# Optimization experiments

Hardware: AMD Instinct MI355X
Metric: run time of the kernel (lower is better)

## Reference

```python
import jax, jax.numpy as jnp
import numpy as np


def _quantize_activation(x):
    """Vectorized equivalent of improved_quantize_activation.

    Original per-element loop: scale by dynamic percentile-based scale, floor,
    clamp to int8 range, take two's-complement 8-bit string, replace the low
    4 bits with '1000', then MSR-4 'compensation' sets the last bit to '1'
    (unconditionally in both branches) -> low nibble becomes 0b1001 = 9.
    Equivalent bit ops: u = (q mod 256) & 0xF0 | 0x09, re-sign, dequantize.
    The torch code detaches (numpy round-trip), so gradients are cut; we
    mirror that with stop_gradient.
    """
    flat = x.reshape(-1)
    abs_max = jnp.maximum(jnp.abs(jnp.percentile(flat, 2.5)),
                          jnp.abs(jnp.percentile(flat, 97.5)))
    scale = jnp.where(abs_max > 0, 127.0 / abs_max, 128.0)
    q = jnp.clip(jnp.floor(x * scale), -128.0, 127.0).astype(jnp.int32)
    u = jnp.mod(q, 256)                      # two's complement byte
    u2 = jnp.bitwise_or(jnp.bitwise_and(u, 0xF0), 9)  # low nibble -> 1001
    s = jnp.where(u2 >= 128, u2 - 256, u2)   # back to signed int8 value
    return jax.lax.stop_gradient(s.astype(x.dtype) / scale)


def _conv2d(x, w, b, pad):
    y = jax.lax.conv_general_dilated(
        x, w, window_strides=(1, 1), padding=[(pad, pad), (pad, pad)],
        dimension_numbers=('NCHW', 'OIHW', 'NCHW'))
    return y + b[None, :, None, None]


def _maxpool2(x):
    return jax.lax.reduce_window(x, -jnp.inf, jax.lax.max,
                                 (1, 1, 2, 2), (1, 1, 2, 2), 'VALID')


def setup_inputs() -> dict:
    key = jax.random.key(0)
    ks = jax.random.split(key, 11)
    B = 16384
    x = jax.random.normal(ks[0], (B, 1, 28, 28), dtype=jnp.float32)
    def u(k, shape, fan_in):
        bound = 1.0 / np.sqrt(fan_in)
        return jax.random.uniform(k, shape, jnp.float32, -bound, bound)
    return {
        'x': x,
        'conv1_w': u(ks[1], (6, 1, 5, 5), 1 * 25),
        'conv1_b': u(ks[2], (6,), 1 * 25),
        'conv2_w': u(ks[3], (16, 6, 5, 5), 6 * 25),
        'conv2_b': u(ks[4], (16,), 6 * 25),
        'fc1_w': u(ks[5], (120, 400), 400),
        'fc1_b': u(ks[6], (120,), 400),
        'fc2_w': u(ks[7], (84, 120), 120),
        'fc2_b': u(ks[8], (84,), 120),
        'fc3_w': u(ks[9], (10, 84), 84),
        'fc3_b': u(ks[10], (10,), 84),
    }


def reference(x, conv1_w, conv1_b, conv2_w, conv2_b,
              fc1_w, fc1_b, fc2_w, fc2_b, fc3_w, fc3_b):
    h = jax.nn.relu(_conv2d(x, conv1_w, conv1_b, pad=2))   # [B,6,28,28]
    h = _maxpool2(h)                                       # [B,6,14,14]
    h = _quantize_activation(h)
    h = jax.nn.relu(_conv2d(h, conv2_w, conv2_b, pad=0))   # [B,16,10,10]
    h = _maxpool2(h)                                       # [B,16,5,5]
    h = _quantize_activation(h)
    h = h.reshape(h.shape[0], -1)                          # [B,400]
    h = jax.nn.relu(h @ fc1_w.T + fc1_b)
    h = _quantize_activation(h)
    # dropout is identity in eval mode
    h = jax.nn.relu(h @ fc2_w.T + fc2_b)
    h = _quantize_activation(h)
    return h @ fc3_w.T + fc3_b                             # [B,10]
```

## Files before the change

### kernel.cpp

```cpp
#include <hip/hip_runtime.h>
#include <stdint.h>
#include <math.h>

#define NB 16384

struct Ctrl {
  unsigned rank[4];
  unsigned key[4];
  float scale;
  unsigned pad[7];
};
static_assert(sizeof(Ctrl) == 64, "ctrl size");

__device__ __forceinline__ unsigned keyOf(float x) {
  unsigned u = __float_as_uint(x);
  return (u & 0x80000000u) ? ~u : (u | 0x80000000u);
}
__device__ __forceinline__ float keyToFloat(unsigned k) {
  unsigned u = (k & 0x80000000u) ? (k ^ 0x80000000u) : ~k;
  return __uint_as_float(u);
}

__global__ __launch_bounds__(256) void conv1_pool(
    const float* __restrict__ x, const float* __restrict__ w,
    const float* __restrict__ bias, float* __restrict__ out) {
  __shared__ float img[784];
  __shared__ float wl[150];
  __shared__ float bl[6];
  int t = threadIdx.x;
  int b = blockIdx.x;
  const float* xb = x + (size_t)b * 784;
  for (int i = t; i < 784; i += 256) img[i] = xb[i];
  if (t < 150) wl[t] = w[t];
  if (t < 6) bl[t] = bias[t];
  __syncthreads();
  for (int o = t; o < 1176; o += 256) {
    int c = o / 196;
    int rem = o % 196;
    int r = rem / 14, col = rem % 14;
    float win[6][6];
    int r0 = 2 * r - 2, c0 = 2 * col - 2;
#pragma unroll
    for (int i = 0; i < 6; i++) {
      int rr = r0 + i;
#pragma unroll
      for (int j = 0; j < 6; j++) {
        int cc = c0 + j;
        win[i][j] = (rr >= 0 && rr < 28 && cc >= 0 && cc < 28) ? img[rr * 28 + cc] : 0.0f;
      }
    }
    float s00 = 0.f, s01 = 0.f, s10 = 0.f, s11 = 0.f;
    const float* wc = &wl[c * 25];
#pragma unroll
    for (int i = 0; i < 5; i++) {
#pragma unroll
      for (int j = 0; j < 5; j++) {
        float wv = wc[i * 5 + j];
        s00 = fmaf(win[i][j], wv, s00);
        s01 = fmaf(win[i][j + 1], wv, s01);
        s10 = fmaf(win[i + 1][j], wv, s10);
        s11 = fmaf(win[i + 1][j + 1], wv, s11);
      }
    }
    float m = fmaxf(fmaxf(s00, s01), fmaxf(s10, s11));
    out[(size_t)b * 1176 + o] = fmaxf(m + bl[c], 0.0f);
  }
}

__global__ __launch_bounds__(256) void conv2_pool(
    const float* __restrict__ a, const float* __restrict__ w,
    const float* __restrict__ bias, float* __restrict__ out) {
  __shared__ float img[1176];
  __shared__ float wl[2400];
  __shared__ float bl[16];
  int t = threadIdx.x;
  int b = blockIdx.x;
  const float* ab = a + (size_t)b * 1176;
  for (int i = t; i < 1176; i += 256) img[i] = ab[i];
  for (int i = t; i < 2400; i += 256) wl[i] = w[i];
  if (t < 16) bl[t] = bias[t];
  __syncthreads();
  for (int o = t; o < 400; o += 256) {
    int c = o / 25;
    int rem = o % 25;
    int r = rem / 5, col = rem % 5;
    float s00 = 0.f, s01 = 0.f, s10 = 0.f, s11 = 0.f;
    for (int ci = 0; ci < 6; ci++) {
      float win[6][6];
      const float* ic = &img[ci * 196 + (2 * r) * 14 + 2 * col];
#pragma unroll
      for (int i = 0; i < 6; i++)
#pragma unroll
        for (int j = 0; j < 6; j++) win[i][j] = ic[i * 14 + j];
      const float* wc = &wl[(c * 6 + ci) * 25];
#pragma unroll
      for (int i = 0; i < 5; i++) {
#pragma unroll
        for (int j = 0; j < 5; j++) {
          float wv = wc[i * 5 + j];
          s00 = fmaf(win[i][j], wv, s00);
          s01 = fmaf(win[i][j + 1], wv, s01);
          s10 = fmaf(win[i + 1][j], wv, s10);
          s11 = fmaf(win[i + 1][j + 1], wv, s11);
        }
      }
    }
    float m = fmaxf(fmaxf(s00, s01), fmaxf(s10, s11));
    out[(size_t)b * 400 + o] = fmaxf(m + bl[c], 0.0f);
  }
}

__global__ __launch_bounds__(256) void hist_top(
    const float4* __restrict__ a, long long n4, unsigned* __restrict__ hist) {
  __shared__ unsigned h[4096];
  int t = threadIdx.x;
  for (int i = t; i < 4096; i += 256) h[i] = 0;
  __syncthreads();
  long long stride = (long long)gridDim.x * 256;
  for (long long i = (long long)blockIdx.x * 256 + t; i < n4; i += stride) {
    float4 v = a[i];
    atomicAdd(&h[keyOf(v.x) >> 20], 1u);
    atomicAdd(&h[keyOf(v.y) >> 20], 1u);
    atomicAdd(&h[keyOf(v.z) >> 20], 1u);
    atomicAdd(&h[keyOf(v.w) >> 20], 1u);
  }
  __syncthreads();
  for (int i = t; i < 4096; i += 256) {
    unsigned v = h[i];
    if (v) atomicAdd(&hist[i], v);
  }
}

__global__ __launch_bounds__(256) void hist_sub(
    const float4* __restrict__ a, long long n4, const Ctrl* __restrict__ c,
    unsigned* __restrict__ hist, int level) {
  __shared__ unsigned h[4096];
  int t = threadIdx.x;
  for (int i = t; i < 4096; i += 256) h[i] = 0;
  __syncthreads();
  unsigned p0 = c->key[0], p1 = c->key[1], p2 = c->key[2], p3 = c->key[3];
  unsigned mask = (level == 2) ? 0xFFF00000u : 0xFFFFFC00u;
  int sh = (level == 2) ? 10 : 0;
  long long stride = (long long)gridDim.x * 256;
  for (long long i = (long long)blockIdx.x * 256 + t; i < n4; i += stride) {
    float4 v = a[i];
    float vals[4] = {v.x, v.y, v.z, v.w};
#pragma unroll
    for (int q = 0; q < 4; q++) {
      unsigned k = keyOf(vals[q]);
      unsigned pf = k & mask;
      unsigned bin = (k >> sh) & 1023u;
      if (pf == p0) atomicAdd(&h[bin], 1u);
      if (pf == p1) atomicAdd(&h[1024 + bin], 1u);
      if (pf == p2) atomicAdd(&h[2048 + bin], 1u);
      if (pf == p3) atomicAdd(&h[3072 + bin], 1u);
    }
  }
  __syncthreads();
  for (int i = t; i < 4096; i += 256) {
    unsigned v = h[i];
    if (v) atomicAdd(&hist[i], v);
  }
}

__global__ __launch_bounds__(256) void scan_step(
    const unsigned* __restrict__ hist, int nbins, int sharedHist, int shift,
    Ctrl* __restrict__ c, int first, unsigned r0, unsigned r1, unsigned r2,
    unsigned r3, int finalize, float lwlo, float hwlo, float lwhi, float hwhi) {
  __shared__ unsigned base[256];
  int t = threadIdx.x;
  unsigned rinit[4] = {r0, r1, r2, r3};
  int per = nbins / 256;
  for (int j = 0; j < 4; j++) {
    const unsigned* h = hist + (sharedHist ? 0 : j * nbins);
    unsigned s = 0;
    for (int i = 0; i < per; i++) s += h[t * per + i];
    base[t] = s;
    __syncthreads();
    if (t == 0) {
      unsigned acc = 0;
      for (int i = 0; i < 256; i++) {
        unsigned v = base[i];
        base[i] = acc;
        acc += v;
      }
    }
    __syncthreads();
    unsigned rank = first ? rinit[j] : c->rank[j];
    unsigned bexc = base[t];
    if (rank >= bexc && rank < bexc + s) {
      unsigned cum = bexc;
      for (int i = 0; i < per; i++) {
        unsigned cnt = h[t * per + i];
        if (rank < cum + cnt) {
          c->rank[j] = rank - cum;
          c->key[j] |= ((unsigned)(t * per + i)) << shift;
          break;
        }
        cum += cnt;
      }
    }
    __syncthreads();
  }
  if (finalize && t == 0) {
    float v0 = keyToFloat(c->key[0]), v1 = keyToFloat(c->key[1]);
    float v2 = keyToFloat(c->key[2]), v3 = keyToFloat(c->key[3]);
    float plo = __fadd_rn(__fmul_rn(v0, lwlo), __fmul_rn(v1, hwlo));
    float phi = __fadd_rn(__fmul_rn(v2, lwhi), __fmul_rn(v3, hwhi));
    float am = fmaxf(fabsf(plo), fabsf(phi));
    c->scale = (am > 0.0f) ? __fdiv_rn(127.0f, am) : 128.0f;
  }
}

__device__ __forceinline__ float qmap1(float x, float scale) {
  float t = __fmul_rn(x, scale);
  t = floorf(t);
  t = fminf(fmaxf(t, -128.0f), 127.0f);
  int qi = (int)t;
  int u2 = (qi & 0xF0) | 9;
  int s = (u2 >= 128) ? (u2 - 256) : u2;
  return __fdiv_rn((float)s, scale);
}

__global__ __launch_bounds__(256) void quant_map(
    float4* __restrict__ a, long long n4, const Ctrl* __restrict__ c) {
  float scale = c->scale;
  long long stride = (long long)gridDim.x * 256;
  for (long long i = (long long)blockIdx.x * 256 + threadIdx.x; i < n4; i += stride) {
    float4 v = a[i];
    v.x = qmap1(v.x, scale);
    v.y = qmap1(v.y, scale);
    v.z = qmap1(v.z, scale);
    v.w = qmap1(v.w, scale);
    a[i] = v;
  }
}

__global__ __launch_bounds__(256) void fc1_kernel(
    const float* __restrict__ A, const float* __restrict__ W,
    const float* __restrict__ bias, float* __restrict__ out) {
  __shared__ float As[32][100];
  __shared__ float Ws[120][100];
  int t = threadIdx.x;
  size_t b0 = (size_t)blockIdx.x * 32;
  int ng = t & 7, bs = t >> 3;
  float acc[15];
#pragma unroll
  for (int i = 0; i < 15; i++) acc[i] = 0.f;
  for (int kc = 0; kc < 4; kc++) {
    for (int idx = t; idx < 3200; idx += 256) {
      int row = idx / 100, k = idx % 100;
      As[row][k] = A[(b0 + row) * 400 + kc * 100 + k];
    }
    for (int idx = t; idx < 12000; idx += 256) {
      int n = idx / 100, k = idx % 100;
      Ws[n][k] = W[n * 400 + kc * 100 + k];
    }
    __syncthreads();
    for (int k = 0; k < 100; k++) {
      float av = As[bs][k];
#pragma unroll
      for (int i = 0; i < 15; i++) acc[i] = fmaf(av, Ws[ng + 8 * i][k], acc[i]);
    }
    __syncthreads();
  }
#pragma unroll
  for (int i = 0; i < 15; i++) {
    int n = ng + 8 * i;
    out[(b0 + bs) * 120 + n] = fmaxf(acc[i] + bias[n], 0.0f);
  }
}

__global__ __launch_bounds__(256) void fc2_kernel(
    const float* __restrict__ A, const float* __restrict__ W,
    const float* __restrict__ bias, float* __restrict__ out) {
  __shared__ float As[64][121];
  __shared__ float Ws[84][120];
  int t = threadIdx.x;
  size_t b0 = (size_t)blockIdx.x * 64;
  int ng = t & 3, bs = t >> 2;
  float acc[21];
#pragma unroll
  for (int i = 0; i < 21; i++) acc[i] = 0.f;
  for (int idx = t; idx < 7680; idx += 256) {
    int row = idx / 120, k = idx % 120;
    As[row][k] = A[(b0 + row) * 120 + k];
  }
  for (int idx = t; idx < 10080; idx += 256) {
    int n = idx / 120, k = idx % 120;
    Ws[n][k] = W[n * 120 + k];
  }
  __syncthreads();
  for (int k = 0; k < 120; k++) {
    float av = As[bs][k];
#pragma unroll
    for (int i = 0; i < 21; i++) acc[i] = fmaf(av, Ws[ng + 4 * i][k], acc[i]);
  }
#pragma unroll
  for (int i = 0; i < 21; i++) {
    int n = ng + 4 * i;
    out[(b0 + bs) * 84 + n] = fmaxf(acc[i] + bias[n], 0.0f);
  }
}

__global__ __launch_bounds__(256) void fc3_kernel(
    const float* __restrict__ A, const float* __restrict__ W,
    const float* __restrict__ bias, float* __restrict__ out) {
  __shared__ float As[64][84];
  __shared__ float Ws[10][84];
  __shared__ float bl[10];
  int t = threadIdx.x;
  size_t b0 = (size_t)blockIdx.x * 64;
  int ng = t & 3, bs = t >> 2;
  for (int idx = t; idx < 5376; idx += 256) {
    int row = idx / 84, k = idx % 84;
    As[row][k] = A[(b0 + row) * 84 + k];
  }
  for (int idx = t; idx < 840; idx += 256) Ws[idx / 84][idx % 84] = W[idx];
  if (t < 10) bl[t] = bias[t];
  __syncthreads();
  float acc[3] = {0.f, 0.f, 0.f};
  for (int k = 0; k < 84; k++) {
    float av = As[bs][k];
#pragma unroll
    for (int i = 0; i < 3; i++) {
      int n = ng + 4 * i;
      if (n < 10) acc[i] = fmaf(av, Ws[n][k], acc[i]);
    }
  }
#pragma unroll
  for (int i = 0; i < 3; i++) {
    int n = ng + 4 * i;
    if (n < 10) out[(b0 + bs) * 10 + n] = acc[i] + bl[n];
  }
}

static void qparams(long long n, unsigned r[4], float w[4]) {
  float nf = (float)n;
  float nm1 = nf - 1.0f;
  float qlo = 2.5f / 100.0f, qhi = 97.5f / 100.0f;
  float ilo = qlo * nm1;
  float flo = floorf(ilo), clo = ceilf(ilo);
  float hwlo = ilo - flo, lwlo = 1.0f - hwlo;
  float ihi = qhi * nm1;
  float fhi = floorf(ihi), chi = ceilf(ihi);
  float hwhi = ihi - fhi, lwhi = 1.0f - hwhi;
  if (flo < 0) flo = 0;
  if (clo < 0) clo = 0;
  if (fhi < 0) fhi = 0;
  if (chi < 0) chi = 0;
  unsigned nmax = (unsigned)(n - 1);
  r[0] = (unsigned)flo; if (r[0] > nmax) r[0] = nmax;
  r[1] = (unsigned)clo; if (r[1] > nmax) r[1] = nmax;
  r[2] = (unsigned)fhi; if (r[2] > nmax) r[2] = nmax;
  r[3] = (unsigned)chi; if (r[3] > nmax) r[3] = nmax;
  w[0] = lwlo; w[1] = hwlo; w[2] = lwhi; w[3] = hwhi;
}

extern "C" void kernel_launch(void* const* d_in, const int* in_sizes, int n_in,
                              void* d_out, int out_size, void* d_ws, size_t ws_size,
                              hipStream_t stream) {
  const float* x   = (const float*)d_in[0];
  const float* c1w = (const float*)d_in[1];
  const float* c1b = (const float*)d_in[2];
  const float* c2w = (const float*)d_in[3];
  const float* c2b = (const float*)d_in[4];
  const float* f1w = (const float*)d_in[5];
  const float* f1b = (const float*)d_in[6];
  const float* f2w = (const float*)d_in[7];
  const float* f2b = (const float*)d_in[8];
  const float* f3w = (const float*)d_in[9];
  const float* f3b = (const float*)d_in[10];
  float* outp = (float*)d_out;

  char* ws = (char*)d_ws;
  size_t off = 0;
  auto alloc = [&](size_t bytes) {
    void* p = ws + off;
    off += (bytes + 255) & ~(size_t)255;
    return p;
  };
  float* act1 = (float*)alloc((size_t)NB * 1176 * 4);
  float* act2 = (float*)alloc((size_t)NB * 400 * 4);
  unsigned* hist1 = (unsigned*)alloc(4096 * 4);
  unsigned* hist2 = (unsigned*)alloc(4096 * 4);
  unsigned* hist3 = (unsigned*)alloc(4096 * 4);
  Ctrl* ctrl = (Ctrl*)alloc(sizeof(Ctrl));
  float* fc1o = act1;
  float* fc2o = act1 + (size_t)NB * 120;

  const int HB = 2048;

  auto runQuant = [&](float* act, long long n) {
    unsigned r[4];
    float w[4];
    qparams(n, r, w);
    hipMemsetAsync(hist1, 0, 3 * 4096 * 4 + sizeof(Ctrl), stream);
    long long n4 = n / 4;
    hist_top<<<HB, 256, 0, stream>>>((const float4*)act, n4, hist1);
    scan_step<<<1, 256, 0, stream>>>(hist1, 4096, 1, 20, ctrl, 1,
                                     r[0], r[1], r[2], r[3], 0, 0.f, 0.f, 0.f, 0.f);
    hist_sub<<<HB, 256, 0, stream>>>((const float4*)act, n4, ctrl, hist2, 2);
    scan_step<<<1, 256, 0, stream>>>(hist2, 1024, 0, 10, ctrl, 0,
                                     0u, 0u, 0u, 0u, 0, 0.f, 0.f, 0.f, 0.f);
    hist_sub<<<HB, 256, 0, stream>>>((const float4*)act, n4, ctrl, hist3, 3);
    scan_step<<<1, 256, 0, stream>>>(hist3, 1024, 0, 0, ctrl, 0,
                                     0u, 0u, 0u, 0u, 1, w[0], w[1], w[2], w[3]);
    quant_map<<<HB, 256, 0, stream>>>((float4*)act, n4, ctrl);
  };

  conv1_pool<<<NB, 256, 0, stream>>>(x, c1w, c1b, act1);
  runQuant(act1, (long long)NB * 1176);
  conv2_pool<<<NB, 256, 0, stream>>>(act1, c2w, c2b, act2);
  runQuant(act2, (long long)NB * 400);
  fc1_kernel<<<NB / 32, 256, 0, stream>>>(act2, f1w, f1b, fc1o);
  runQuant(fc1o, (long long)NB * 120);
  fc2_kernel<<<NB / 64, 256, 0, stream>>>(fc1o, f2w, f2b, fc2o);
  runQuant(fc2o, (long long)NB * 84);
  fc3_kernel<<<NB / 64, 256, 0, stream>>>(fc2o, f3w, f3b, outp);
}
```

Baseline: 1.082 ms.

## Fuse quantile histograms, scans and quant-map into conv/fc kernels with last-block scans

The top-level histogram is now built inside the producing conv/fc kernels, and each scan runs in the last block to finish, found through an atomic counter. This removes separate histogram and scan launches. The quantize-map pass is folded into the consumer kernel's input load, so there is no extra read/write pass over each activation. The conv kernels are also restructured: several images per block, padded shared tiles, two channels per thread in conv1, and register-blocked rows with transposed weights in conv2. Zero values are counted separately to avoid atomic contention on the many ReLU zeros. The cost is heavier kernels with more shared memory and last-block serialization of the scans.

```diff
diff --git a/kernel.cpp b/kernel.cpp
--- a/kernel.cpp
+++ b/kernel.cpp
@@ -20,198 +20,6 @@
   unsigned u = (k & 0x80000000u) ? (k ^ 0x80000000u) : ~k;
   return __uint_as_float(u);
 }
-
-__global__ __launch_bounds__(256) void conv1_pool(
-    const float* __restrict__ x, const float* __restrict__ w,
-    const float* __restrict__ bias, float* __restrict__ out) {
-  __shared__ float img[784];
-  __shared__ float wl[150];
-  __shared__ float bl[6];
-  int t = threadIdx.x;
-  int b = blockIdx.x;
-  const float* xb = x + (size_t)b * 784;
-  for (int i = t; i < 784; i += 256) img[i] = xb[i];
-  if (t < 150) wl[t] = w[t];
-  if (t < 6) bl[t] = bias[t];
-  __syncthreads();
-  for (int o = t; o < 1176; o += 256) {
-    int c = o / 196;
-    int rem = o % 196;
-    int r = rem / 14, col = rem % 14;
-    float win[6][6];
-    int r0 = 2 * r - 2, c0 = 2 * col - 2;
-#pragma unroll
-    for (int i = 0; i < 6; i++) {
-      int rr = r0 + i;
-#pragma unroll
-      for (int j = 0; j < 6; j++) {
-        int cc = c0 + j;
-        win[i][j] = (rr >= 0 && rr < 28 && cc >= 0 && cc < 28) ? img[rr * 28 + cc] : 0.0f;
-      }
-    }
-    float s00 = 0.f, s01 = 0.f, s10 = 0.f, s11 = 0.f;
-    const float* wc = &wl[c * 25];
-#pragma unroll
-    for (int i = 0; i < 5; i++) {
-#pragma unroll
-      for (int j = 0; j < 5; j++) {
-        float wv = wc[i * 5 + j];
-        s00 = fmaf(win[i][j], wv, s00);
-        s01 = fmaf(win[i][j + 1], wv, s01);
-        s10 = fmaf(win[i + 1][j], wv, s10);
-        s11 = fmaf(win[i + 1][j + 1], wv, s11);
-      }
-    }
-    float m = fmaxf(fmaxf(s00, s01), fmaxf(s10, s11));
-    out[(size_t)b * 1176 + o] = fmaxf(m + bl[c], 0.0f);
-  }
-}
-
-__global__ __launch_bounds__(256) void conv2_pool(
-    const float* __restrict__ a, const float* __restrict__ w,
-    const float* __restrict__ bias, float* __restrict__ out) {
-  __shared__ float img[1176];
-  __shared__ float wl[2400];
-  __shared__ float bl[16];
-  int t = threadIdx.x;
-  int b = blockIdx.x;
-  const float* ab = a + (size_t)b * 1176;
-  for (int i = t; i < 1176; i += 256) img[i] = ab[i];
-  for (int i = t; i < 2400; i += 256) wl[i] = w[i];
-  if (t < 16) bl[t] = bias[t];
-  __syncthreads();
-  for (int o = t; o < 400; o += 256) {
-    int c = o / 25;
-    int rem = o % 25;
-    int r = rem / 5, col = rem % 5;
-    float s00 = 0.f, s01 = 0.f, s10 = 0.f, s11 = 0.f;
-    for (int ci = 0; ci < 6; ci++) {
-      float win[6][6];
-      const float* ic = &img[ci * 196 + (2 * r) * 14 + 2 * col];
-#pragma unroll
-      for (int i = 0; i < 6; i++)
-#pragma unroll
-        for (int j = 0; j < 6; j++) win[i][j] = ic[i * 14 + j];
-      const float* wc = &wl[(c * 6 + ci) * 25];
-#pragma unroll
-      for (int i = 0; i < 5; i++) {
-#pragma unroll
-        for (int j = 0; j < 5; j++) {
-          float wv = wc[i * 5 + j];
-          s00 = fmaf(win[i][j], wv, s00);
-          s01 = fmaf(win[i][j + 1], wv, s01);
-          s10 = fmaf(win[i + 1][j], wv, s10);
-          s11 = fmaf(win[i + 1][j + 1], wv, s11);
-        }
-      }
-    }
-    float m = fmaxf(fmaxf(s00, s01), fmaxf(s10, s11));
-    out[(size_t)b * 400 + o] = fmaxf(m + bl[c], 0.0f);
-  }
-}
-
-__global__ __launch_bounds__(256) void hist_top(
-    const float4* __restrict__ a, long long n4, unsigned* __restrict__ hist) {
-  __shared__ unsigned h[4096];
-  int t = threadIdx.x;
-  for (int i = t; i < 4096; i += 256) h[i] = 0;
-  __syncthreads();
-  long long stride = (long long)gridDim.x * 256;
-  for (long long i = (long long)blockIdx.x * 256 + t; i < n4; i += stride) {
-    float4 v = a[i];
-    atomicAdd(&h[keyOf(v.x) >> 20], 1u);
-    atomicAdd(&h[keyOf(v.y) >> 20], 1u);
-    atomicAdd(&h[keyOf(v.z) >> 20], 1u);
-    atomicAdd(&h[keyOf(v.w) >> 20], 1u);
-  }
-  __syncthreads();
-  for (int i = t; i < 4096; i += 256) {
-    unsigned v = h[i];
-    if (v) atomicAdd(&hist[i], v);
-  }
-}
-
-__global__ __launch_bounds__(256) void hist_sub(
-    const float4* __restrict__ a, long long n4, const Ctrl* __restrict__ c,
-    unsigned* __restrict__ hist, int level) {
-  __shared__ unsigned h[4096];
-  int t = threadIdx.x;
-  for (int i = t; i < 4096; i += 256) h[i] = 0;
-  __syncthreads();
-  unsigned p0 = c->key[0], p1 = c->key[1], p2 = c->key[2], p3 = c->key[3];
-  unsigned mask = (level == 2) ? 0xFFF00000u : 0xFFFFFC00u;
-  int sh = (level == 2) ? 10 : 0;
-  long long stride = (long long)gridDim.x * 256;
-  for (long long i = (long long)blockIdx.x * 256 + t; i < n4; i += stride) {
-    float4 v = a[i];
-    float vals[4] = {v.x, v.y, v.z, v.w};
-#pragma unroll
-    for (int q = 0; q < 4; q++) {
-      unsigned k = keyOf(vals[q]);
-      unsigned pf = k & mask;
-      unsigned bin = (k >> sh) & 1023u;
-      if (pf == p0) atomicAdd(&h[bin], 1u);
-      if (pf == p1) atomicAdd(&h[1024 + bin], 1u);
-      if (pf == p2) atomicAdd(&h[2048 + bin], 1u);
-      if (pf == p3) atomicAdd(&h[3072 + bin], 1u);
-    }
-  }
-  __syncthreads();
-  for (int i = t; i < 4096; i += 256) {
-    unsigned v = h[i];
-    if (v) atomicAdd(&hist[i], v);
-  }
-}
-
-__global__ __launch_bounds__(256) void scan_step(
-    const unsigned* __restrict__ hist, int nbins, int sharedHist, int shift,
-    Ctrl* __restrict__ c, int first, unsigned r0, unsigned r1, unsigned r2,
-    unsigned r3, int finalize, float lwlo, float hwlo, float lwhi, float hwhi) {
-  __shared__ unsigned base[256];
-  int t = threadIdx.x;
-  unsigned rinit[4] = {r0, r1, r2, r3};
-  int per = nbins / 256;
-  for (int j = 0; j < 4; j++) {
-    const unsigned* h = hist + (sharedHist ? 0 : j * nbins);
-    unsigned s = 0;
-    for (int i = 0; i < per; i++) s += h[t * per + i];
-    base[t] = s;
-    __syncthreads();
-    if (t == 0) {
-      unsigned acc = 0;
-      for (int i = 0; i < 256; i++) {
-        unsigned v = base[i];
-        base[i] = acc;
-        acc += v;
-      }
-    }
-    __syncthreads();
-    unsigned rank = first ? rinit[j] : c->rank[j];
-    unsigned bexc = base[t];
-    if (rank >= bexc && rank < bexc + s) {
-      unsigned cum = bexc;
-      for (int i = 0; i < per; i++) {
-        unsigned cnt = h[t * per + i];
-        if (rank < cum + cnt) {
-          c->rank[j] = rank - cum;
-          c->key[j] |= ((unsigned)(t * per + i)) << shift;
-          break;
-        }
-        cum += cnt;
-      }
-    }
-    __syncthreads();
-  }
-  if (finalize && t == 0) {
-    float v0 = keyToFloat(c->key[0]), v1 = keyToFloat(c->key[1]);
-    float v2 = keyToFloat(c->key[2]), v3 = keyToFloat(c->key[3]);
-    float plo = __fadd_rn(__fmul_rn(v0, lwlo), __fmul_rn(v1, hwlo));
-    float phi = __fadd_rn(__fmul_rn(v2, lwhi), __fmul_rn(v3, hwhi));
-    float am = fmaxf(fabsf(plo), fabsf(phi));
-    c->scale = (am > 0.0f) ? __fdiv_rn(127.0f, am) : 128.0f;
-  }
-}
-
 __device__ __forceinline__ float qmap1(float x, float scale) {
   float t = __fmul_rn(x, scale);
   t = floorf(t);
@@ -221,36 +29,328 @@
   int s = (u2 >= 128) ? (u2 - 256) : u2;
   return __fdiv_rn((float)s, scale);
 }
-
-__global__ __launch_bounds__(256) void quant_map(
-    float4* __restrict__ a, long long n4, const Ctrl* __restrict__ c) {
-  float scale = c->scale;
+__device__ __forceinline__ unsigned loadAgent(const unsigned* p) {
+  return __hip_atomic_load(p, __ATOMIC_RELAXED, __HIP_MEMORY_SCOPE_AGENT);
+}
+__device__ __forceinline__ void load16(float* r, const float* p) {
+#pragma unroll
+  for (int s = 0; s < 4; s++) {
+    float4 f = *(const float4*)&p[4 * s];
+    r[4 * s] = f.x; r[4 * s + 1] = f.y; r[4 * s + 2] = f.z; r[4 * s + 3] = f.w;
+  }
+}
+
+__device__ void scan_device(const unsigned* hist, int nbins, int sharedHist, int shift,
+                            Ctrl* c, int first, unsigned r0, unsigned r1, unsigned r2,
+                            unsigned r3, int finalize, float lwlo, float hwlo,
+                            float lwhi, float hwhi, unsigned* base) {
+  int t = threadIdx.x;
+  unsigned rinit[4] = {r0, r1, r2, r3};
+  int per = nbins / 256;
+  for (int j = 0; j < 4; j++) {
+    const unsigned* h = hist + (sharedHist ? 0 : j * nbins);
+    unsigned s = 0;
+    for (int i = 0; i < per; i++) s += loadAgent(&h[t * per + i]);
+    base[t] = s;
+    __syncthreads();
+    if (t == 0) {
+      unsigned acc = 0;
+      for (int i = 0; i < 256; i++) { unsigned v = base[i]; base[i] = acc; acc += v; }
+    }
+    __syncthreads();
+    unsigned rank = first ? rinit[j] : c->rank[j];
+    unsigned bexc = base[t];
+    if (rank >= bexc && rank < bexc + s) {
+      unsigned cum = bexc;
+      for (int i = 0; i < per; i++) {
+        unsigned cnt = loadAgent(&h[t * per + i]);
+        if (rank < cum + cnt) {
+          c->rank[j] = rank - cum;
+          c->key[j] |= ((unsigned)(t * per + i)) << shift;
+          break;
+        }
+        cum += cnt;
+      }
+    }
+    __syncthreads();
+  }
+  if (finalize && t == 0) {
+    float v0 = keyToFloat(c->key[0]), v1 = keyToFloat(c->key[1]);
+    float v2 = keyToFloat(c->key[2]), v3 = keyToFloat(c->key[3]);
+    float plo = __fadd_rn(__fmul_rn(v0, lwlo), __fmul_rn(v1, hwlo));
+    float phi = __fadd_rn(__fmul_rn(v2, lwhi), __fmul_rn(v3, hwhi));
+    float am = fmaxf(fabsf(plo), fabsf(phi));
+    c->scale = (am > 0.0f) ? __fdiv_rn(127.0f, am) : 128.0f;
+  }
+}
+
+#define C1_IMGS 6
+__global__ __launch_bounds__(256) void conv1_fused(
+    const float* __restrict__ x, const float* __restrict__ w,
+    const float* __restrict__ bias, float* __restrict__ act1,
+    unsigned* __restrict__ hist, unsigned* __restrict__ counter, Ctrl* ctrl,
+    unsigned r0, unsigned r1, unsigned r2, unsigned r3) {
+  __shared__ __align__(16) float img[C1_IMGS * 1032];
+  __shared__ float wl[150];
+  __shared__ float bl[6];
+  __shared__ unsigned h[4096];
+  __shared__ unsigned sbase[256];
+  __shared__ unsigned lastFlag;
+  int t = threadIdx.x;
+  long long b0 = (long long)blockIdx.x * C1_IMGS;
+  for (int i = t; i < 4096; i += 256) h[i] = 0;
+  if (t < 150) wl[t] = w[t];
+  if (t < 6) bl[t] = bias[t];
+  for (int i = t; i < C1_IMGS * 1032; i += 256) img[i] = 0.0f;
+  __syncthreads();
+  for (int idx = t; idx < C1_IMGS * 784; idx += 256) {
+    int im = idx / 784, rem = idx % 784;
+    int r = rem / 28, cc = rem % 28;
+    long long bb = b0 + im;
+    if (bb < NB) img[im * 1032 + (r + 2) * 32 + (cc + 2)] = x[bb * 784 + rem];
+  }
+  __syncthreads();
+  unsigned zc = 0;
+  int im = t / 42, rem2 = t % 42, cg = rem2 / 14, pc = rem2 % 14;
+  if (im < C1_IMGS) {
+    long long bb = b0 + im;
+    if (bb < NB) {
+      const float* ib = &img[im * 1032];
+      float wa[25], wb[25];
+#pragma unroll
+      for (int k = 0; k < 25; k++) {
+        wa[k] = wl[(2 * cg) * 25 + k];
+        wb[k] = wl[(2 * cg + 1) * 25 + k];
+      }
+      float biasA = bl[2 * cg], biasB = bl[2 * cg + 1];
+      float* oA = act1 + bb * 1176 + (2 * cg) * 196 + pc;
+      float* oB = oA + 196;
+      for (int pr = 0; pr < 14; pr++) {
+        float rw[6][6];
+        const float* rp = ib + (2 * pr) * 32 + 2 * pc;
+#pragma unroll
+        for (int rr = 0; rr < 6; rr++) {
+#pragma unroll
+          for (int k2 = 0; k2 < 3; k2++) {
+            float2 f = *(const float2*)&rp[rr * 32 + 2 * k2];
+            rw[rr][2 * k2] = f.x;
+            rw[rr][2 * k2 + 1] = f.y;
+          }
+        }
+        float a00 = 0.f, a01 = 0.f, a10 = 0.f, a11 = 0.f;
+        float c00 = 0.f, c01 = 0.f, c10 = 0.f, c11 = 0.f;
+#pragma unroll
+        for (int i = 0; i < 5; i++) {
+#pragma unroll
+          for (int j = 0; j < 5; j++) {
+            float wva = wa[i * 5 + j], wvb = wb[i * 5 + j];
+            a00 = fmaf(rw[i][j], wva, a00);
+            a01 = fmaf(rw[i][j + 1], wva, a01);
+            a10 = fmaf(rw[i + 1][j], wva, a10);
+            a11 = fmaf(rw[i + 1][j + 1], wva, a11);
+            c00 = fmaf(rw[i][j], wvb, c00);
+            c01 = fmaf(rw[i][j + 1], wvb, c01);
+            c10 = fmaf(rw[i + 1][j], wvb, c10);
+            c11 = fmaf(rw[i + 1][j + 1], wvb, c11);
+          }
+        }
+        float ma = fmaxf(fmaxf(a00, a01), fmaxf(a10, a11));
+        float mb = fmaxf(fmaxf(c00, c01), fmaxf(c10, c11));
+        float va = fmaxf(ma + biasA, 0.0f);
+        float vb = fmaxf(mb + biasB, 0.0f);
+        oA[pr * 14] = va;
+        oB[pr * 14] = vb;
+        unsigned ba = __float_as_uint(va), bbit = __float_as_uint(vb);
+        if (ba == 0u) zc++; else atomicAdd(&h[keyOf(va) >> 20], 1u);
+        if (bbit == 0u) zc++; else atomicAdd(&h[keyOf(vb) >> 20], 1u);
+      }
+    }
+  }
+  if (zc) atomicAdd(&h[2048], zc);
+  __syncthreads();
+  for (int i = t; i < 4096; i += 256) {
+    unsigned v = h[i];
+    if (v) atomicAdd(&hist[i], v);
+  }
+  __threadfence();
+  if (t == 0) lastFlag = (atomicAdd(counter, 1u) == gridDim.x - 1);
+  __syncthreads();
+  if (lastFlag)
+    scan_device(hist, 4096, 1, 20, ctrl, 1, r0, r1, r2, r3, 0, 0.f, 0.f, 0.f, 0.f, sbase);
+}
+
+#define C2_IMGS 3
+__global__ __launch_bounds__(256) void conv2_fused(
+    const float* __restrict__ act1, const float* __restrict__ w,
+    const float* __restrict__ bias, const Ctrl* __restrict__ cin,
+    float* __restrict__ act2, unsigned* __restrict__ hist,
+    unsigned* __restrict__ counter, Ctrl* ctrl,
+    unsigned r0, unsigned r1, unsigned r2, unsigned r3) {
+  __shared__ __align__(16) float img[C2_IMGS * 1680];
+  __shared__ float wl[2400];
+  __shared__ float bl[16];
+  __shared__ unsigned h[4096];
+  __shared__ unsigned sbase[256];
+  __shared__ unsigned lastFlag;
+  int t = threadIdx.x;
+  long long b0 = (long long)blockIdx.x * C2_IMGS;
+  float scale = cin->scale;
+  for (int i = t; i < 4096; i += 256) h[i] = 0;
+  for (int idx = t; idx < 2400; idx += 256) {
+    int c = idx / 150, rem = idx % 150;
+    int ci = rem / 25, ki = (rem % 25) / 5, kj = rem % 5;
+    wl[((ci * 5 + ki) * 5 + kj) * 16 + c] = w[idx];
+  }
+  if (t < 16) bl[t] = bias[t];
+  for (int idx = t; idx < C2_IMGS * 1176; idx += 256) {
+    int im = idx / 1176, rem = idx % 1176;
+    int ci = rem / 196, rr = (rem % 196) / 14, cc = rem % 14;
+    long long bb = b0 + im;
+    float v = 0.0f;
+    if (bb < NB) v = qmap1(act1[bb * 1176 + rem], scale);
+    img[im * 1680 + ci * 280 + rr * 20 + cc] = v;
+  }
+  __syncthreads();
+  unsigned zc = 0;
+  int g = t >> 4;
+  int c = t & 15;
+  if (g < 15) {
+    int im = g / 5, pr = g % 5;
+    long long bb = b0 + im;
+    if (bb < NB) {
+      const float* ib = &img[im * 1680];
+      float acc0[10], acc1[10];
+#pragma unroll
+      for (int i = 0; i < 10; i++) { acc0[i] = 0.f; acc1[i] = 0.f; }
+      for (int ci = 0; ci < 6; ci++) {
+        const float* rbase = ib + ci * 280 + (2 * pr) * 20;
+        float ra[16], rb[16];
+        load16(ra, rbase);
+        load16(rb, rbase + 20);
+#pragma unroll
+        for (int ki = 0; ki < 5; ki++) {
+          float wv[5];
+#pragma unroll
+          for (int kj = 0; kj < 5; kj++) wv[kj] = wl[((ci * 5 + ki) * 5 + kj) * 16 + c];
+#pragma unroll
+          for (int kj = 0; kj < 5; kj++) {
+            float wvv = wv[kj];
+#pragma unroll
+            for (int col = 0; col < 10; col++) {
+              acc0[col] = fmaf(ra[col + kj], wvv, acc0[col]);
+              acc1[col] = fmaf(rb[col + kj], wvv, acc1[col]);
+            }
+          }
+          if (ki < 4) {
+#pragma unroll
+            for (int q = 0; q < 16; q++) ra[q] = rb[q];
+            load16(rb, rbase + (ki + 2) * 20);
+          }
+        }
+      }
+      float bv = bl[c];
+      float* op = act2 + ((bb * 16 + c) * 5 + pr) * 5;
+#pragma unroll
+      for (int p = 0; p < 5; p++) {
+        float m = fmaxf(fmaxf(acc0[2 * p], acc0[2 * p + 1]),
+                        fmaxf(acc1[2 * p], acc1[2 * p + 1]));
+        float v = fmaxf(m + bv, 0.0f);
+        op[p] = v;
+        unsigned bits = __float_as_uint(v);
+        if (bits == 0u) zc++; else atomicAdd(&h[keyOf(v) >> 20], 1u);
+      }
+    }
+  }
+  if (zc) atomicAdd(&h[2048], zc);
+  __syncthreads();
+  for (int i = t; i < 4096; i += 256) {
+    unsigned v = h[i];
+    if (v) atomicAdd(&hist[i], v);
+  }
+  __threadfence();
+  if (t == 0) lastFlag = (atomicAdd(counter, 1u) == gridDim.x - 1);
+  __syncthreads();
+  if (lastFlag)
+    scan_device(hist, 4096, 1, 20, ctrl, 1, r0, r1, r2, r3, 0, 0.f, 0.f, 0.f, 0.f, sbase);
+}
+
+__global__ __launch_bounds__(256) void sub_fused(
+    const float4* __restrict__ a, long long n4, Ctrl* c,
+    unsigned* __restrict__ histOut, int level, unsigned* __restrict__ counter,
+    int finalize, float lwlo, float hwlo, float lwhi, float hwhi) {
+  __shared__ unsigned h[4096];
+  __shared__ unsigned sbase[256];
+  __shared__ unsigned lastFlag;
+  int t = threadIdx.x;
+  for (int i = t; i < 4096; i += 256) h[i] = 0;
+  __syncthreads();
+  unsigned p0 = c->key[0], p1 = c->key[1], p2 = c->key[2], p3 = c->key[3];
+  unsigned mask = (level == 2) ? 0xFFF00000u : 0xFFFFFC00u;
+  int sh = (level == 2) ? 10 : 0;
+  const unsigned zkey = 0x80000000u;
+  int zm0 = ((zkey & mask) == p0), zm1 = ((zkey & mask) == p1);
+  int zm2 = ((zkey & mask) == p2), zm3 = ((zkey & mask) == p3);
+  unsigned zbin = (zkey >> sh) & 1023u;
+  unsigned zc = 0;
   long long stride = (long long)gridDim.x * 256;
-  for (long long i = (long long)blockIdx.x * 256 + threadIdx.x; i < n4; i += stride) {
+  for (long long i = (long long)blockIdx.x * 256 + t; i < n4; i += stride) {
     float4 v = a[i];
-    v.x = qmap1(v.x, scale);
-    v.y = qmap1(v.y, scale);
-    v.z = qmap1(v.z, scale);
-    v.w = qmap1(v.w, scale);
-    a[i] = v;
-  }
-}
-
-__global__ __launch_bounds__(256) void fc1_kernel(
+    float vals[4] = {v.x, v.y, v.z, v.w};
+#pragma unroll
+    for (int q = 0; q < 4; q++) {
+      unsigned bits = __float_as_uint(vals[q]);
+      if (bits == 0u) { zc++; continue; }
+      unsigned k = keyOf(vals[q]);
+      unsigned pf = k & mask;
+      unsigned bin = (k >> sh) & 1023u;
+      if (pf == p0) atomicAdd(&h[bin], 1u);
+      if (pf == p1) atomicAdd(&h[1024 + bin], 1u);
+      if (pf == p2) atomicAdd(&h[2048 + bin], 1u);
+      if (pf == p3) atomicAdd(&h[3072 + bin], 1u);
+    }
+  }
+  if (zc) {
+    if (zm0) atomicAdd(&h[zbin], zc);
+    if (zm1) atomicAdd(&h[1024 + zbin], zc);
+    if (zm2) atomicAdd(&h[2048 + zbin], zc);
+    if (zm3) atomicAdd(&h[3072 + zbin], zc);
+  }
+  __syncthreads();
+  for (int i = t; i < 4096; i += 256) {
+    unsigned v = h[i];
+    if (v) atomicAdd(&histOut[i], v);
+  }
+  __threadfence();
+  if (t == 0) lastFlag = (atomicAdd(counter, 1u) == gridDim.x - 1);
+  __syncthreads();
+  if (lastFlag)
+    scan_device(histOut, 1024, 0, sh, c, 0, 0u, 0u, 0u, 0u, finalize, lwlo, hwlo, lwhi, hwhi, sbase);
+}
+
+__global__ __launch_bounds__(256) void fc1_fused(
     const float* __restrict__ A, const float* __restrict__ W,
-    const float* __restrict__ bias, float* __restrict__ out) {
+    const float* __restrict__ bias, const Ctrl* __restrict__ cin,
+    float* __restrict__ out, unsigned* __restrict__ hist,
+    unsigned* __restrict__ counter, Ctrl* ctrl,
+    unsigned r0, unsigned r1, unsigned r2, unsigned r3) {
   __shared__ float As[32][100];
   __shared__ float Ws[120][100];
+  __shared__ unsigned h[4096];
+  __shared__ unsigned sbase[256];
+  __shared__ unsigned lastFlag;
   int t = threadIdx.x;
   size_t b0 = (size_t)blockIdx.x * 32;
+  float scale = cin->scale;
+  for (int i = t; i < 4096; i += 256) h[i] = 0;
   int ng = t & 7, bs = t >> 3;
   float acc[15];
 #pragma unroll
   for (int i = 0; i < 15; i++) acc[i] = 0.f;
   for (int kc = 0; kc < 4; kc++) {
+    __syncthreads();
     for (int idx = t; idx < 3200; idx += 256) {
       int row = idx / 100, k = idx % 100;
-      As[row][k] = A[(b0 + row) * 400 + kc * 100 + k];
+      As[row][k] = qmap1(A[(b0 + row) * 400 + kc * 100 + k], scale);
     }
     for (int idx = t; idx < 12000; idx += 256) {
       int n = idx / 100, k = idx % 100;
@@ -262,29 +362,51 @@
 #pragma unroll
       for (int i = 0; i < 15; i++) acc[i] = fmaf(av, Ws[ng + 8 * i][k], acc[i]);
     }
-    __syncthreads();
-  }
+  }
+  unsigned zc = 0;
 #pragma unroll
   for (int i = 0; i < 15; i++) {
     int n = ng + 8 * i;
-    out[(b0 + bs) * 120 + n] = fmaxf(acc[i] + bias[n], 0.0f);
-  }
-}
-
-__global__ __launch_bounds__(256) void fc2_kernel(
+    float v = fmaxf(acc[i] + bias[n], 0.0f);
+    out[(b0 + bs) * 120 + n] = v;
+    unsigned bits = __float_as_uint(v);
+    if (bits == 0u) zc++; else atomicAdd(&h[keyOf(v) >> 20], 1u);
+  }
+  if (zc) atomicAdd(&h[2048], zc);
+  __syncthreads();
+  for (int i = t; i < 4096; i += 256) {
+    unsigned v = h[i];
+    if (v) atomicAdd(&hist[i], v);
+  }
+  __threadfence();
+  if (t == 0) lastFlag = (atomicAdd(counter, 1u) == gridDim.x - 1);
+  __syncthreads();
+  if (lastFlag)
+    scan_device(hist, 4096, 1, 20, ctrl, 1, r0, r1, r2, r3, 0, 0.f, 0.f, 0.f, 0.f, sbase);
+}
+
+__global__ __launch_bounds__(256) void fc2_fused(
     const float* __restrict__ A, const float* __restrict__ W,
-    const float* __restrict__ bias, float* __restrict__ out) {
+    const float* __restrict__ bias, const Ctrl* __restrict__ cin,
+    float* __restrict__ out, unsigned* __restrict__ hist,
+    unsigned* __restrict__ counter, Ctrl* ctrl,
+    unsigned r0, unsigned r1, unsigned r2, unsigned r3) {
   __shared__ float As[64][121];
   __shared__ float Ws[84][120];
+  __shared__ unsigned h[4096];
+  __shared__ unsigned sbase[256];
+  __shared__ unsigned lastFlag;
   int t = threadIdx.x;
   size_t b0 = (size_t)blockIdx.x * 64;
+  float scale = cin->scale;
+  for (int i = t; i < 4096; i += 256) h[i] = 0;
   int ng = t & 3, bs = t >> 2;
   float acc[21];
 #pragma unroll
   for (int i = 0; i < 21; i++) acc[i] = 0.f;
   for (int idx = t; idx < 7680; idx += 256) {
     int row = idx / 120, k = idx % 120;
-    As[row][k] = A[(b0 + row) * 120 + k];
+    As[row][k] = qmap1(A[(b0 + row) * 120 + k], scale);
   }
   for (int idx = t; idx < 10080; idx += 256) {
     int n = idx / 120, k = idx % 120;
@@ -296,25 +418,42 @@
 #pragma unroll
     for (int i = 0; i < 21; i++) acc[i] = fmaf(av, Ws[ng + 4 * i][k], acc[i]);
   }
+  unsigned zc = 0;
 #pragma unroll
   for (int i = 0; i < 21; i++) {
     int n = ng + 4 * i;
-    out[(b0 + bs) * 84 + n] = fmaxf(acc[i] + bias[n], 0.0f);
-  }
-}
-
-__global__ __launch_bounds__(256) void fc3_kernel(
+    float v = fmaxf(acc[i] + bias[n], 0.0f);
+    out[(b0 + bs) * 84 + n] = v;
+    unsigned bits = __float_as_uint(v);
+    if (bits == 0u) zc++; else atomicAdd(&h[keyOf(v) >> 20], 1u);
+  }
+  if (zc) atomicAdd(&h[2048], zc);
+  __syncthreads();
+  for (int i = t; i < 4096; i += 256) {
+    unsigned v = h[i];
+    if (v) atomicAdd(&hist[i], v);
+  }
+  __threadfence();
+  if (t == 0) lastFlag = (atomicAdd(counter, 1u) == gridDim.x - 1);
+  __syncthreads();
+  if (lastFlag)
+    scan_device(hist, 4096, 1, 20, ctrl, 1, r0, r1, r2, r3, 0, 0.f, 0.f, 0.f, 0.f, sbase);
+}
+
+__global__ __launch_bounds__(256) void fc3_fused(
     const float* __restrict__ A, const float* __restrict__ W,
-    const float* __restrict__ bias, float* __restrict__ out) {
+    const float* __restrict__ bias, const Ctrl* __restrict__ cin,
+    float* __restrict__ out) {
   __shared__ float As[64][84];
   __shared__ float Ws[10][84];
   __shared__ float bl[10];
   int t = threadIdx.x;
   size_t b0 = (size_t)blockIdx.x * 64;
+  float scale = cin->scale;
   int ng = t & 3, bs = t >> 2;
   for (int idx = t; idx < 5376; idx += 256) {
     int row = idx / 84, k = idx % 84;
-    As[row][k] = A[(b0 + row) * 84 + k];
+    As[row][k] = qmap1(A[(b0 + row) * 84 + k], scale);
   }
   for (int idx = t; idx < 840; idx += 256) Ws[idx / 84][idx % 84] = W[idx];
   if (t < 10) bl[t] = bias[t];
@@ -382,40 +521,53 @@
   };
   float* act1 = (float*)alloc((size_t)NB * 1176 * 4);
   float* act2 = (float*)alloc((size_t)NB * 400 * 4);
-  unsigned* hist1 = (unsigned*)alloc(4096 * 4);
-  unsigned* hist2 = (unsigned*)alloc(4096 * 4);
-  unsigned* hist3 = (unsigned*)alloc(4096 * 4);
-  Ctrl* ctrl = (Ctrl*)alloc(sizeof(Ctrl));
+  unsigned* meta = (unsigned*)alloc(4 * 12288 * 4 + 16 * 4 + 4 * sizeof(Ctrl));
+  unsigned* cnt = meta + 4 * 12288;
+  Ctrl* ctrl = (Ctrl*)(cnt + 16);
   float* fc1o = act1;
   float* fc2o = act1 + (size_t)NB * 120;
 
-  const int HB = 2048;
-
-  auto runQuant = [&](float* act, long long n) {
-    unsigned r[4];
-    float w[4];
-    qparams(n, r, w);
-    hipMemsetAsync(hist1, 0, 3 * 4096 * 4 + sizeof(Ctrl), stream);
-    long long n4 = n / 4;
-    hist_top<<<HB, 256, 0, stream>>>((const float4*)act, n4, hist1);
-    scan_step<<<1, 256, 0, stream>>>(hist1, 4096, 1, 20, ctrl, 1,
-                                     r[0], r[1], r[2], r[3], 0, 0.f, 0.f, 0.f, 0.f);
-    hist_sub<<<HB, 256, 0, stream>>>((const float4*)act, n4, ctrl, hist2, 2);
-    scan_step<<<1, 256, 0, stream>>>(hist2, 1024, 0, 10, ctrl, 0,
-                                     0u, 0u, 0u, 0u, 0, 0.f, 0.f, 0.f, 0.f);
-    hist_sub<<<HB, 256, 0, stream>>>((const float4*)act, n4, ctrl, hist3, 3);
-    scan_step<<<1, 256, 0, stream>>>(hist3, 1024, 0, 0, ctrl, 0,
-                                     0u, 0u, 0u, 0u, 1, w[0], w[1], w[2], w[3]);
-    quant_map<<<HB, 256, 0, stream>>>((float4*)act, n4, ctrl);
+  auto H = [&](int s, int lvl) {
+    return meta + s * 12288 + (lvl == 1 ? 0 : (lvl == 2 ? 4096 : 8192));
   };
 
-  conv1_pool<<<NB, 256, 0, stream>>>(x, c1w, c1b, act1);
-  runQuant(act1, (long long)NB * 1176);
-  conv2_pool<<<NB, 256, 0, stream>>>(act1, c2w, c2b, act2);
-  runQuant(act2, (long long)NB * 400);
-  fc1_kernel<<<NB / 32, 256, 0, stream>>>(act2, f1w, f1b, fc1o);
-  runQuant(fc1o, (long long)NB * 120);
-  fc2_kernel<<<NB / 64, 256, 0, stream>>>(fc1o, f2w, f2b, fc2o);
-  runQuant(fc2o, (long long)NB * 84);
-  fc3_kernel<<<NB / 64, 256, 0, stream>>>(fc2o, f3w, f3b, outp);
-}
+  long long n1 = (long long)NB * 1176, n2 = (long long)NB * 400;
+  long long n3 = (long long)NB * 120, n4n = (long long)NB * 84;
+  unsigned r1[4], r2[4], r3[4], r4[4];
+  float w1[4], w2[4], w3[4], w4[4];
+  qparams(n1, r1, w1);
+  qparams(n2, r2, w2);
+  qparams(n3, r3, w3);
+  qparams(n4n, r4, w4);
+
+  hipMemsetAsync(meta, 0, 4 * 12288 * 4 + 16 * 4 + 4 * sizeof(Ctrl), stream);
+
+  int g1 = (NB + C1_IMGS - 1) / C1_IMGS;
+  int g2 = (NB + C2_IMGS - 1) / C2_IMGS;
+
+  conv1_fused<<<g1, 256, 0, stream>>>(x, c1w, c1b, act1, H(0, 1), &cnt[0], &ctrl[0],
+                                      r1[0], r1[1], r1[2], r1[3]);
+  sub_fused<<<2048, 256, 0, stream>>>((const float4*)act1, n1 / 4, &ctrl[0], H(0, 2), 2,
+                                      &cnt[1], 0, 0.f, 0.f, 0.f, 0.f);
+  sub_fused<<<2048, 256, 0, stream>>>((const float4*)act1, n1 / 4, &ctrl[0], H(0, 3), 3,
+                                      &cnt[2], 1, w1[0], w1[1], w1[2], w1[3]);
+  conv2_fused<<<g2, 256, 0, stream>>>(act1, c2w, c2b, &ctrl[0], act2, H(1, 1), &cnt[3],
+                                      &ctrl[1], r2[0], r2[1], r2[2], r2[3]);
+  sub_fused<<<2048, 256, 0, stream>>>((const float4*)act2, n2 / 4, &ctrl[1], H(1, 2), 2,
+                                      &cnt[4], 0, 0.f, 0.f, 0.f, 0.f);
+  sub_fused<<<2048, 256, 0, stream>>>((const float4*)act2, n2 / 4, &ctrl[1], H(1, 3), 3,
+                                      &cnt[5], 1, w2[0], w2[1], w2[2], w2[3]);
+  fc1_fused<<<NB / 32, 256, 0, stream>>>(act2, f1w, f1b, &ctrl[1], fc1o, H(2, 1), &cnt[6],
+                                         &ctrl[2], r3[0], r3[1], r3[2], r3[3]);
+  sub_fused<<<512, 256, 0, stream>>>((const float4*)fc1o, n3 / 4, &ctrl[2], H(2, 2), 2,
+                                     &cnt[7], 0, 0.f, 0.f, 0.f, 0.f);
+  sub_fused<<<512, 256, 0, stream>>>((const float4*)fc1o, n3 / 4, &ctrl[2], H(2, 3), 3,
+                                     &cnt[8], 1, w3[0], w3[1], w3[2], w3[3]);
+  fc2_fused<<<NB / 64, 256, 0, stream>>>(fc1o, f2w, f2b, &ctrl[2], fc2o, H(3, 1), &cnt[9],
+                                         &ctrl[3], r4[0], r4[1], r4[2], r4[3]);
+  sub_fused<<<512, 256, 0, stream>>>((const float4*)fc2o, n4n / 4, &ctrl[3], H(3, 2), 2,
+                                     &cnt[10], 0, 0.f, 0.f, 0.f, 0.f);
+  sub_fused<<<512, 256, 0, stream>>>((const float4*)fc2o, n4n / 4, &ctrl[3], H(3, 3), 3,
+                                     &cnt[11], 1, w4[0], w4[1], w4[2], w4[3]);
+  fc3_fused<<<NB / 64, 256, 0, stream>>>(fc2o, f3w, f3b, &ctrl[3], outp);
+}
```

Result: slower. 2.246 ms (+107.6%).
